# Optimization experiments

Measured on AMD Instinct MI355X. Metric: run time of the kernel, lower is better.

## Reference

```python
import jax, jax.numpy as jnp
import numpy as np

B, S, H, E, K = 4, 4096, 1024, 8, 2


def setup_inputs() -> dict:
    key = jax.random.key(0)
    ks = jax.random.split(key, 5)
    scale = 1.0 / np.sqrt(H)
    return {
        "x": jax.random.normal(ks[0], (B, S, H), dtype=jnp.float32),
        "gate_w": jax.random.normal(ks[1], (H, E), dtype=jnp.float32) * scale,
        "gate_b": jnp.zeros((E,), dtype=jnp.float32),
        "expert_w": jax.random.normal(ks[2], (E, H, H), dtype=jnp.float32) * scale,
        "expert_b": jnp.zeros((E, H), dtype=jnp.float32),
    }


def reference(x, gate_w, gate_b, expert_w, expert_b):
    bsz, seq_len, hsz = x.shape
    h = x.reshape(-1, hsz)                              # [T, H], T = B*S

    # --- router ---
    router_logits = h @ gate_w + gate_b                 # [T, E]
    probs = jax.nn.softmax(router_logits, axis=-1)
    top_w, top_idx = jax.lax.top_k(probs, K)            # [T, K]
    top_w = top_w / jnp.sum(top_w, axis=-1, keepdims=True)

    # combine weight per (token, expert): sum over top-k slots of w * onehot(idx)
    one_hot = jax.nn.one_hot(top_idx, E, dtype=h.dtype)  # [T, K, E]
    combine = jnp.einsum("tk,tke->te", top_w, one_hot)   # [T, E]

    # --- experts (dense grouped GEMM, masked-combined; same math as gather/scatter loop) ---
    expert_out = jnp.einsum("th,ehd->etd", h, expert_w) + expert_b[:, None, :]  # [E, T, H]
    out = jnp.einsum("te,etd->td", combine, expert_out)                          # [T, H]

    return out.reshape(bsz, seq_len, hsz), router_logits
```

## Files before the change

### kernel.cpp

```cpp
#include <hip/hip_runtime.h>

#define TT 16384
#define HH 1024
#define EE 8

typedef __attribute__((ext_vector_type(8))) short short8;
typedef __attribute__((ext_vector_type(4))) float f32x4;

__device__ inline unsigned short f2bf(float f) {
    union { float f; unsigned int u; } v; v.f = f;
    unsigned int u = v.u;
    unsigned int r = (u + 0x7FFFu + ((u >> 16) & 1u)) >> 16;
    return (unsigned short)r;
}

__global__ __launch_bounds__(256) void transpose_w_kernel(
    const float* __restrict__ w, unsigned short* __restrict__ wt)
{
    __shared__ unsigned short tile[64][66];
    int bid = blockIdx.x;
    int e   = bid >> 8;
    int rem = bid & 255;
    int hb  = ((rem >> 4) & 15) * 64;
    int db  = (rem & 15) * 64;
    int tid = threadIdx.x;
    int c4  = (tid & 15) * 4;
    int r0  = tid >> 4;

    const float* we = w + (size_t)e * HH * HH;
    #pragma unroll
    for (int i = 0; i < 4; ++i) {
        int r = i * 16 + r0;
        float4 v = *(const float4*)(we + (size_t)(hb + r) * HH + db + c4);
        tile[r][c4 + 0] = f2bf(v.x);
        tile[r][c4 + 1] = f2bf(v.y);
        tile[r][c4 + 2] = f2bf(v.z);
        tile[r][c4 + 3] = f2bf(v.w);
    }
    __syncthreads();
    unsigned short* wte = wt + (size_t)e * HH * HH;
    #pragma unroll
    for (int i = 0; i < 4; ++i) {
        int dr = i * 16 + r0;
        ushort4 o;
        o.x = tile[c4 + 0][dr];
        o.y = tile[c4 + 1][dr];
        o.z = tile[c4 + 2][dr];
        o.w = tile[c4 + 3][dr];
        *(ushort4*)(wte + (size_t)(db + dr) * HH + hb + c4) = o;
    }
}

__global__ __launch_bounds__(256) void router_logits_kernel(
    const float* __restrict__ x, const float* __restrict__ gw,
    const float* __restrict__ gb, float* __restrict__ logits,
    int* __restrict__ tops_i, float* __restrict__ tops_w)
{
    __shared__ float gwt[EE][HH];
    int tid = threadIdx.x;
    for (int i = tid; i < (HH * EE) / 4; i += 256) {
        float4 v = ((const float4*)gw)[i];
        int b4 = i * 4;
        gwt[(b4 + 0) & 7][(b4 + 0) >> 3] = v.x;
        gwt[(b4 + 1) & 7][(b4 + 1) >> 3] = v.y;
        gwt[(b4 + 2) & 7][(b4 + 2) >> 3] = v.z;
        gwt[(b4 + 3) & 7][(b4 + 3) >> 3] = v.w;
    }
    __syncthreads();

    const int lane = tid & 63;
    const int wv   = tid >> 6;
    const int t    = blockIdx.x * 4 + wv;
    const float* xrow = x + (size_t)t * HH;

    float4 v0 = *(const float4*)(xrow + 0 * 256 + lane * 4);
    float4 v1 = *(const float4*)(xrow + 1 * 256 + lane * 4);
    float4 v2 = *(const float4*)(xrow + 2 * 256 + lane * 4);
    float4 v3 = *(const float4*)(xrow + 3 * 256 + lane * 4);

    float acc[8];
    #pragma unroll
    for (int e = 0; e < 8; ++e) {
        float4 g0 = *(const float4*)(&gwt[e][0 * 256 + lane * 4]);
        float4 g1 = *(const float4*)(&gwt[e][1 * 256 + lane * 4]);
        float4 g2 = *(const float4*)(&gwt[e][2 * 256 + lane * 4]);
        float4 g3 = *(const float4*)(&gwt[e][3 * 256 + lane * 4]);
        acc[e] = v0.x * g0.x + v0.y * g0.y + v0.z * g0.z + v0.w * g0.w
               + v1.x * g1.x + v1.y * g1.y + v1.z * g1.z + v1.w * g1.w
               + v2.x * g2.x + v2.y * g2.y + v2.z * g2.z + v2.w * g2.w
               + v3.x * g3.x + v3.y * g3.y + v3.z * g3.z + v3.w * g3.w;
    }
    #pragma unroll
    for (int e = 0; e < 8; ++e) {
        #pragma unroll
        for (int off = 32; off >= 1; off >>= 1)
            acc[e] += __shfl_xor(acc[e], off, 64);
    }
    float lg[8];
    #pragma unroll
    for (int e = 0; e < 8; ++e) lg[e] = acc[e] + gb[e];

    float myv = 0.0f;
    #pragma unroll
    for (int e = 0; e < 8; ++e) myv = (lane == e) ? lg[e] : myv;
    if (lane < 8) logits[(size_t)t * EE + lane] = myv;

    int i0 = 0;
    #pragma unroll
    for (int e = 1; e < 8; ++e) if (lg[e] > lg[i0]) i0 = e;
    int i1 = (i0 == 0) ? 1 : 0;
    #pragma unroll
    for (int e = 0; e < 8; ++e) if (e != i0 && lg[e] > lg[i1]) i1 = e;

    float w0 = 1.0f / (1.0f + expf(lg[i1] - lg[i0]));

    if (lane == 0) {
        tops_i[t] = i0 | (i1 << 3);
        tops_w[t] = w0;
    }
}

__global__ __launch_bounds__(256) void build_lists_kernel(
    const int* __restrict__ tops_i, const float* __restrict__ tops_w,
    int* __restrict__ counts, int* __restrict__ tokl, float* __restrict__ wl)
{
    __shared__ int lcnt[EE];
    __shared__ int gbase[EE];
    int tid = threadIdx.x;
    if (tid < EE) lcnt[tid] = 0;
    __syncthreads();

    int t   = blockIdx.x * 256 + tid;
    int rec = tops_i[t];
    int i0  = rec & 7;
    int i1  = (rec >> 3) & 7;
    float w0 = tops_w[t];
    float w1 = 1.0f - w0;

    int r0 = atomicAdd(&lcnt[i0], 1);
    int r1 = atomicAdd(&lcnt[i1], 1);
    __syncthreads();

    if (tid < EE) gbase[tid] = atomicAdd(&counts[tid], lcnt[tid]);
    __syncthreads();

    int p0 = gbase[i0] + r0;
    tokl[i0 * TT + p0] = t; wl[i0 * TT + p0] = w0;
    int p1 = gbase[i1] + r1;
    tokl[i1 * TT + p1] = t; wl[i1 * TT + p1] = w1;
}

__global__ __launch_bounds__(256) void stream_init_kernel(
    const float* __restrict__ x, const float* __restrict__ eb,
    const int* __restrict__ tops_i, const float* __restrict__ tops_w,
    unsigned short* __restrict__ xb, float* __restrict__ out)
{
    const int N4 = TT * HH / 4;
    int stride = gridDim.x * 256;
    for (int f = blockIdx.x * 256 + threadIdx.x; f < N4; f += stride) {
        int t  = f >> 8;
        int c4 = f & 255;
        int rec = tops_i[t];
        int i0  = rec & 7;
        int i1  = (rec >> 3) & 7;
        float w0 = tops_w[t];
        float w1 = 1.0f - w0;

        float4 v = ((const float4*)x)[f];
        ushort4 bv;
        bv.x = f2bf(v.x); bv.y = f2bf(v.y); bv.z = f2bf(v.z); bv.w = f2bf(v.w);
        ((ushort4*)xb)[f] = bv;

        float4 a = *(const float4*)(eb + (size_t)i0 * HH + c4 * 4);
        float4 c = *(const float4*)(eb + (size_t)i1 * HH + c4 * 4);
        float4 r;
        r.x = w0 * a.x + w1 * c.x;
        r.y = w0 * a.y + w1 * c.y;
        r.z = w0 * a.z + w1 * c.z;
        r.w = w0 * a.w + w1 * c.w;
        ((float4*)out)[f] = r;
    }
}

#define BM 128
#define BN 128
#define BK 64

__global__ __launch_bounds__(256) void moe_gemm_kernel(
    const unsigned short* __restrict__ xb, const unsigned short* __restrict__ wt,
    const int* __restrict__ counts, const int* __restrict__ tokl,
    const float* __restrict__ wl, float* __restrict__ out)
{
    int bid = blockIdx.x;
    int e   = bid & 7;
    int j   = bid >> 3;
    int mb  = j >> 3;
    int nb  = j & 7;
    int cnt = counts[e];
    int row0 = mb * BM;
    if (row0 >= cnt) return;

    __shared__ __align__(16) unsigned short Alds[BM * BK];
    __shared__ __align__(16) unsigned short Blds[BN * BK];
    __shared__ int   toks[BM];
    __shared__ float wgts[BM];

    int tid = threadIdx.x;
    if (tid < BM) {
        int g = row0 + tid;
        bool ok = g < cnt;
        toks[tid] = ok ? tokl[e * TT + g] : 0;
        wgts[tid] = ok ? wl[e * TT + g] : 0.0f;
    }
    __syncthreads();

    const int lane = tid & 63;
    const int wv   = tid >> 6;
    const int wr   = wv >> 1, wc = wv & 1;
    const int mrow = wr * 64, ncol = wc * 64;

    f32x4 acc[4][4];
    #pragma unroll
    for (int m = 0; m < 4; ++m)
        #pragma unroll
        for (int n = 0; n < 4; ++n) acc[m][n] = (f32x4)0.0f;

    const unsigned short* wte = wt + (size_t)e * HH * HH + (size_t)(nb * BN) * HH;
    const int off = wv * 1024 + lane * 16;

    const unsigned short* abase[4];
    const unsigned short* bbase[4];
    #pragma unroll
    for (int rnd = 0; rnd < 4; ++rnd) {
        int o  = rnd * 4096 + off;
        int r  = o >> 7;
        int cb = (o & 127) >> 1;
        abase[rnd] = xb + (size_t)toks[r] * HH + cb;
        bbase[rnd] = wte + (size_t)r * HH + cb;
    }

    for (int kt = 0; kt < HH / BK; ++kt) {
        int k0 = kt * BK;
        #pragma unroll
        for (int rnd = 0; rnd < 4; ++rnd) {
            __builtin_amdgcn_global_load_lds(
                (const __attribute__((address_space(1))) void*)(abase[rnd] + k0),
                (__attribute__((address_space(3))) void*)((char*)Alds + rnd * 4096 + wv * 1024),
                16, 0, 0);
            __builtin_amdgcn_global_load_lds(
                (const __attribute__((address_space(1))) void*)(bbase[rnd] + k0),
                (__attribute__((address_space(3))) void*)((char*)Blds + rnd * 4096 + wv * 1024),
                16, 0, 0);
        }
        __syncthreads();
        #pragma unroll
        for (int kk = 0; kk < 2; ++kk) {
            int kb = kk * 64 + (lane >> 4) * 16;
            short8 av[4], bv[4];
            #pragma unroll
            for (int m = 0; m < 4; ++m)
                av[m] = *(const short8*)((const char*)Alds + (mrow + m * 16 + (lane & 15)) * 128 + kb);
            #pragma unroll
            for (int n = 0; n < 4; ++n)
                bv[n] = *(const short8*)((const char*)Blds + (ncol + n * 16 + (lane & 15)) * 128 + kb);
            #pragma unroll
            for (int m = 0; m < 4; ++m)
                #pragma unroll
                for (int n = 0; n < 4; ++n)
                    acc[m][n] = __builtin_amdgcn_mfma_f32_16x16x32_bf16(av[m], bv[n], acc[m][n], 0, 0, 0);
        }
        __syncthreads();
    }

    #pragma unroll
    for (int m = 0; m < 4; ++m) {
        int lr0 = mrow + m * 16 + ((lane >> 4) << 2);
        #pragma unroll
        for (int rg = 0; rg < 4; ++rg) {
            int lr = lr0 + rg;
            int tkn = toks[lr];
            float wg = wgts[lr];
            if (wg != 0.0f) {
                float* orow = out + (size_t)tkn * HH + nb * BN + ncol + (lane & 15);
                #pragma unroll
                for (int n = 0; n < 4; ++n)
                    atomicAdd(orow + n * 16, wg * acc[m][n][rg]);
            }
        }
    }
}

extern "C" void kernel_launch(void* const* d_in, const int* in_sizes, int n_in,
                              void* d_out, int out_size, void* d_ws, size_t ws_size,
                              hipStream_t stream) {
    const float* x  = (const float*)d_in[0];
    const float* gw = (const float*)d_in[1];
    const float* gb = (const float*)d_in[2];
    const float* ew = (const float*)d_in[3];
    const float* eb = (const float*)d_in[4];
    float* out    = (float*)d_out;
    float* logits = out + (size_t)TT * HH;

    char* w = (char*)d_ws;
    unsigned short* xb = (unsigned short*)w;
    unsigned short* wt = (unsigned short*)(w + (size_t)TT * HH * 2);
    char* p  = w + (size_t)TT * HH * 2 + (size_t)EE * HH * HH * 2;
    int*   counts = (int*)p;
    int*   tokl   = (int*)(p + 256);
    float* wl     = (float*)(p + 256 + (size_t)EE * TT * 4);
    int*   tops_i = (int*)(p + 256 + 2 * (size_t)EE * TT * 4);
    float* tops_w = (float*)(p + 256 + 2 * (size_t)EE * TT * 4 + TT * 4);

    hipMemsetAsync(counts, 0, 256, stream);
    hipLaunchKernelGGL(transpose_w_kernel, dim3(EE * 256), dim3(256), 0, stream, ew, wt);
    hipLaunchKernelGGL(router_logits_kernel, dim3(TT / 4), dim3(256), 0, stream,
                       x, gw, gb, logits, tops_i, tops_w);
    hipLaunchKernelGGL(build_lists_kernel, dim3(TT / 256), dim3(256), 0, stream,
                       tops_i, tops_w, counts, tokl, wl);
    hipLaunchKernelGGL(stream_init_kernel, dim3(2048), dim3(256), 0, stream,
                       x, eb, tops_i, tops_w, xb, out);
    hipLaunchKernelGGL(moe_gemm_kernel, dim3(EE * (TT / BM) * (HH / BN)), dim3(256), 0, stream,
                       xb, wt, counts, tokl, wl, out);
}
```

Before: 364.3 us.

## Double-buffer MoE GEMM LDS tiles with async global-to-LDS prefetch

```diff
diff --git a/kernel.cpp b/kernel.cpp
--- a/kernel.cpp
+++ b/kernel.cpp
@@ -184,7 +184,8 @@
 
 #define BM 128
 #define BN 128
-#define BK 64
+#define BK 32
+#define NT (HH / BK)
 
 __global__ __launch_bounds__(256) void moe_gemm_kernel(
     const unsigned short* __restrict__ xb, const unsigned short* __restrict__ wt,
@@ -200,8 +201,8 @@
     int row0 = mb * BM;
     if (row0 >= cnt) return;
 
-    __shared__ __align__(16) unsigned short Alds[BM * BK];
-    __shared__ __align__(16) unsigned short Blds[BN * BK];
+    __shared__ __align__(16) unsigned short Alds[2][BM * BK];
+    __shared__ __align__(16) unsigned short Blds[2][BN * BK];
     __shared__ int   toks[BM];
     __shared__ float wgts[BM];
 
@@ -226,51 +227,85 @@
         for (int n = 0; n < 4; ++n) acc[m][n] = (f32x4)0.0f;
 
     const unsigned short* wte = wt + (size_t)e * HH * HH + (size_t)(nb * BN) * HH;
-    const int off = wv * 1024 + lane * 16;
-
-    const unsigned short* abase[4];
-    const unsigned short* bbase[4];
-    #pragma unroll
-    for (int rnd = 0; rnd < 4; ++rnd) {
-        int o  = rnd * 4096 + off;
-        int r  = o >> 7;
-        int cb = (o & 127) >> 1;
-        abase[rnd] = xb + (size_t)toks[r] * HH + cb;
-        bbase[rnd] = wte + (size_t)r * HH + cb;
-    }
-
-    for (int kt = 0; kt < HH / BK; ++kt) {
-        int k0 = kt * BK;
-        #pragma unroll
-        for (int rnd = 0; rnd < 4; ++rnd) {
-            __builtin_amdgcn_global_load_lds(
-                (const __attribute__((address_space(1))) void*)(abase[rnd] + k0),
-                (__attribute__((address_space(3))) void*)((char*)Alds + rnd * 4096 + wv * 1024),
-                16, 0, 0);
-            __builtin_amdgcn_global_load_lds(
-                (const __attribute__((address_space(1))) void*)(bbase[rnd] + k0),
-                (__attribute__((address_space(3))) void*)((char*)Blds + rnd * 4096 + wv * 1024),
-                16, 0, 0);
+
+    const int srow = tid >> 2;
+    const int scol = (tid & 3) * 8;
+    const unsigned short* abase0 = xb + (size_t)toks[srow] * HH + scol;
+    const unsigned short* abase1 = xb + (size_t)toks[srow + 64] * HH + scol;
+    const unsigned short* bbase0 = wte + (size_t)srow * HH + scol;
+    const unsigned short* bbase1 = wte + (size_t)(srow + 64) * HH + scol;
+    const int ldst = tid * 16;
+
+#define STAGE(buf, k0)                                                         \
+    {                                                                          \
+        __builtin_amdgcn_global_load_lds(                                      \
+            (const __attribute__((address_space(1))) void*)(abase0 + (k0)),    \
+            (__attribute__((address_space(3))) void*)((char*)&Alds[buf][0] + ldst), \
+            16, 0, 0);                                                         \
+        __builtin_amdgcn_global_load_lds(                                      \
+            (const __attribute__((address_space(1))) void*)(abase1 + (k0)),    \
+            (__attribute__((address_space(3))) void*)((char*)&Alds[buf][0] + ldst + 4096), \
+            16, 0, 0);                                                         \
+        __builtin_amdgcn_global_load_lds(                                      \
+            (const __attribute__((address_space(1))) void*)(bbase0 + (k0)),    \
+            (__attribute__((address_space(3))) void*)((char*)&Blds[buf][0] + ldst), \
+            16, 0, 0);                                                         \
+        __builtin_amdgcn_global_load_lds(                                      \
+            (const __attribute__((address_space(1))) void*)(bbase1 + (k0)),    \
+            (__attribute__((address_space(3))) void*)((char*)&Blds[buf][0] + ldst + 4096), \
+            16, 0, 0);                                                         \
+    }
+
+#define COMPUTE(buf)                                                           \
+    {                                                                          \
+        int kb = (lane >> 4) * 16;                                             \
+        short8 av[4], bv[4];                                                   \
+        _Pragma("unroll")                                                      \
+        for (int m = 0; m < 4; ++m)                                            \
+            av[m] = *(const short8*)((const char*)&Alds[buf][0] + (mrow + m * 16 + (lane & 15)) * 64 + kb); \
+        _Pragma("unroll")                                                      \
+        for (int n = 0; n < 4; ++n)                                            \
+            bv[n] = *(const short8*)((const char*)&Blds[buf][0] + (ncol + n * 16 + (lane & 15)) * 64 + kb); \
+        _Pragma("unroll")                                                      \
+        for (int m = 0; m < 4; ++m)                                            \
+            _Pragma("unroll")                                                  \
+            for (int n = 0; n < 4; ++n)                                        \
+                acc[m][n] = __builtin_amdgcn_mfma_f32_16x16x32_bf16(av[m], bv[n], acc[m][n], 0, 0, 0); \
+    }
+
+    STAGE(0, 0);
+
+    for (int kt = 0; kt < NT - 1; kt += 2) {
+        STAGE(1, (kt + 1) * BK);
+        asm volatile("s_waitcnt vmcnt(4)" ::: "memory");
+        __builtin_amdgcn_sched_barrier(0);
+        __builtin_amdgcn_s_barrier();
+        __builtin_amdgcn_sched_barrier(0);
+        COMPUTE(0);
+        __builtin_amdgcn_sched_barrier(0);
+        __builtin_amdgcn_s_barrier();
+        __builtin_amdgcn_sched_barrier(0);
+        if (kt + 2 < NT) {
+            STAGE(0, (kt + 2) * BK);
+            asm volatile("s_waitcnt vmcnt(4)" ::: "memory");
+        } else {
+            asm volatile("s_waitcnt vmcnt(0)" ::: "memory");
         }
-        __syncthreads();
-        #pragma unroll
-        for (int kk = 0; kk < 2; ++kk) {
-            int kb = kk * 64 + (lane >> 4) * 16;
-            short8 av[4], bv[4];
-            #pragma unroll
-            for (int m = 0; m < 4; ++m)
-                av[m] = *(const short8*)((const char*)Alds + (mrow + m * 16 + (lane & 15)) * 128 + kb);
-            #pragma unroll
-            for (int n = 0; n < 4; ++n)
-                bv[n] = *(const short8*)((const char*)Blds + (ncol + n * 16 + (lane & 15)) * 128 + kb);
-            #pragma unroll
-            for (int m = 0; m < 4; ++m)
-                #pragma unroll
-                for (int n = 0; n < 4; ++n)
-                    acc[m][n] = __builtin_amdgcn_mfma_f32_16x16x32_bf16(av[m], bv[n], acc[m][n], 0, 0, 0);
-        }
-        __syncthreads();
-    }
+        __builtin_amdgcn_sched_barrier(0);
+        __builtin_amdgcn_s_barrier();
+        __builtin_amdgcn_sched_barrier(0);
+        COMPUTE(1);
+        __builtin_amdgcn_sched_barrier(0);
+        __builtin_amdgcn_s_barrier();
+        __builtin_amdgcn_sched_barrier(0);
+    }
+    {
+        asm volatile("s_waitcnt vmcnt(0)" ::: "memory");
+        __builtin_amdgcn_sched_barrier(0);
+    }
+
+#undef STAGE
+#undef COMPUTE
 
     #pragma unroll
     for (int m = 0; m < 4; ++m) {
```

After: 333.4 us. 8.5% less time.
